# Performance work log

Hardware: AMD Instinct MI355X
Metric: run time of the kernel (lower is better)

The kernel has to match this reference:

```python
import jax, jax.numpy as jnp
import numpy as np

NUM_HEADS = 16


def setup_inputs() -> dict:
    rng = jax.random.key(0)
    ks = jax.random.split(rng, 11)
    T, B, E = 1024, 4, 1024
    s = E ** -0.5  # weight init scale
    return {
        "query": jax.random.normal(ks[0], (T, B, E), jnp.float32),
        "key": jax.random.normal(ks[1], (T, B, E), jnp.float32),
        "value": jax.random.normal(ks[2], (T, B, E), jnp.float32),
        "q_proj_weight": jax.random.normal(ks[3], (E, E), jnp.float32) * s,
        "k_proj_weight1": jax.random.normal(ks[4], (E, E), jnp.float32) * s,
        "k_proj_weight2": jax.random.normal(ks[5], (E, E), jnp.float32) * s,
        "v_proj_weight": jax.random.normal(ks[6], (E, E), jnp.float32) * s,
        "in_proj_bias": jax.random.normal(ks[7], (4 * E,), jnp.float32) * 0.02,
        "out_proj_weight": jax.random.normal(ks[8], (E, E), jnp.float32) * s,
        "out_proj_bias": jax.random.normal(ks[9], (E,), jnp.float32) * 0.02,
        "pi": jax.random.uniform(ks[10], (2, NUM_HEADS), jnp.float32, 0.3, 0.7),
    }


def reference(query, key, value, q_proj_weight, k_proj_weight1, k_proj_weight2,
              v_proj_weight, in_proj_bias, out_proj_weight, out_proj_bias, pi):
    T, Bz, E = query.shape
    H = NUM_HEADS
    hd = E // H
    scaling = hd ** -0.5

    b_q, b_k1, b_k2, b_v = jnp.split(in_proj_bias, 4)
    q = query @ q_proj_weight.T + b_q
    k1 = key @ k_proj_weight1.T + b_k1
    k2 = key @ k_proj_weight2.T + b_k2
    v = value @ v_proj_weight.T + b_v

    def heads(x):  # (S, B, E) -> (B*H, S, hd)
        S = x.shape[0]
        return x.reshape(S, Bz * H, hd).transpose(1, 0, 2)

    q, k1, k2, v = heads(q), heads(k1), heads(k2), heads(v)

    def sqdist(a, b):  # (B*H, Nt, hd), (B*H, Ns, hd) -> (B*H, Nt, Ns)
        a2 = jnp.sum(a * a, axis=-1)
        b2 = jnp.sum(b * b, axis=-1)
        ab = jnp.einsum('btd,bsd->bts', a, b)
        return a2[:, :, None] + b2[:, None, :] - 2.0 * ab

    e1 = jnp.exp(-scaling / 2.0 * sqdist(q, k1))
    e2 = jnp.exp(-3.0 * scaling / 2.0 * sqdist(q, k2))

    pi1 = jnp.clip(jnp.abs(pi[0]), 1e-6, 2.0)  # (H,)
    pi2 = jnp.clip(jnp.abs(pi[1]), 1e-6, 2.0)

    Nt, Ns = e1.shape[1], e1.shape[2]
    attn = (e1.reshape(Bz, H, Nt, Ns) * pi1[None, :, None, None]
            + e2.reshape(Bz, H, Nt, Ns) * pi2[None, :, None, None])
    attn = attn.reshape(Bz * H, Nt, Ns)
    attn = attn / (jnp.sum(attn, axis=-1, keepdims=True) + 1e-6)

    out = jnp.einsum('bts,bsd->btd', attn, v)        # (B*H, Nt, hd)
    out = out.transpose(1, 0, 2).reshape(T, Bz, E)   # (T, B, E)
    return out @ out_proj_weight.T + out_proj_bias
```

## Files before the change

### kernel.cpp

```cpp
#include <hip/hip_runtime.h>
#include <hip/hip_bf16.h>

#define T_DIM 1024
#define B_DIM 4
#define E_DIM 1024
#define H_DIM 16
#define HD    64
#define M_DIM (T_DIM * B_DIM)

typedef __hip_bfloat16 bf16;
typedef __bf16 bf16x8 __attribute__((ext_vector_type(8)));
typedef __bf16 bf16x4 __attribute__((ext_vector_type(4)));
typedef __bf16 bf16x2 __attribute__((ext_vector_type(2)));
typedef float  f32x4  __attribute__((ext_vector_type(4)));

#define P4S ((size_t)M_DIM * E_DIM)
#define P1S ((size_t)E_DIM * E_DIM)

__global__ __launch_bounds__(256) void cvt_all(
    const float* __restrict__ q, const float* __restrict__ k,
    const float* __restrict__ v, const float* __restrict__ w0,
    const float* __restrict__ w1, const float* __restrict__ w2,
    const float* __restrict__ w3, const float* __restrict__ w4,
    __bf16* __restrict__ dst)
{
  size_t i = ((size_t)blockIdx.x * 256 + threadIdx.x) * 8;
  const float* src;
  size_t off;
  if (i < P4S)            { src = q; off = i; }
  else if (i < 2 * P4S)   { src = k; off = i - P4S; }
  else if (i < 3 * P4S)   { src = v; off = i - 2 * P4S; }
  else {
    size_t j = i - 3 * P4S;
    int wsel = (int)(j >> 20);
    off = j & (P1S - 1);
    const float* ws[5] = {w0, w1, w2, w3, w4};
    src = ws[wsel];
  }
  float4 a = *(const float4*)(src + off);
  float4 b = *(const float4*)(src + off + 4);
  bf16x8 o;
  o[0] = (__bf16)a.x; o[1] = (__bf16)a.y; o[2] = (__bf16)a.z; o[3] = (__bf16)a.w;
  o[4] = (__bf16)b.x; o[5] = (__bf16)b.y; o[6] = (__bf16)b.z; o[7] = (__bf16)b.w;
  *(bf16x8*)(dst + i) = o;
}

__device__ __forceinline__ void load_lds16(const __bf16* g, __bf16* l) {
  __builtin_amdgcn_global_load_lds(
      (__attribute__((address_space(1))) void*)(void*)g,
      (__attribute__((address_space(3))) void*)l, 16, 0, 0);
}

__device__ __forceinline__ void stage_half(
    int H, const __bf16* __restrict__ X, const __bf16* __restrict__ W,
    int bm, int bn, __bf16* As, __bf16* Bs, int tid)
{
  if (H >= 64) return;
  const int T  = H >> 2;
  const int h  = H & 3;
  const int rh = (h & 1) * 128;
  const __bf16* src = (h < 2) ? X : W;
  const int rbase   = (h < 2) ? bm : bn;
  __bf16* lb = ((h < 2) ? As : Bs) + (T & 1) * 16384;
#pragma unroll
  for (int li = 0; li < 2; ++li) {
    int r  = rh + li * 64 + (tid >> 3);
    int gc = (tid & 7) ^ (r & 7);
    load_lds16(src + (size_t)(rbase + r) * E_DIM + T * 64 + gc * 8,
               lb + (rh + li * 64) * 64 + tid * 8);
  }
}

#define RD(base, row, c) \
  (*(const bf16x8*)((base) + (row) * 64 + ((((c) ^ ((row) & 7))) << 3)))

__global__ __launch_bounds__(512, 2) void proj_gemm4(
    const __bf16* __restrict__ xbase, const __bf16* __restrict__ wbase,
    const float* __restrict__ bin, __bf16* __restrict__ cbase,
    float* __restrict__ qn_g, float* __restrict__ knr_g)
{
  __shared__ __bf16 lds[65536];
  __bf16* As = lds;
  __bf16* Bs = lds + 32768;

  const int z = blockIdx.z;
  const __bf16* X = xbase + ((z == 0) ? 0 : (z == 3) ? 2 * P4S : P4S);
  const __bf16* W = wbase + (size_t)z * P1S;
  const float* bias = bin + z * E_DIM;
  __bf16* C = cbase + (size_t)z * P4S;

  const int bm = blockIdx.x * 256;
  const int bn = blockIdx.y * 256;

  const int tid  = threadIdx.x;
  const int lane = tid & 63;
  const int w    = tid >> 6;
  const int wm   = w >> 2;
  const int wn   = w & 3;
  const int mrow = lane & 15, quad = lane >> 4;

  f32x4 acc[8][4];
#pragma unroll
  for (int m = 0; m < 8; ++m)
#pragma unroll
    for (int n = 0; n < 4; ++n) acc[m][n] = (f32x4)0.0f;

#pragma unroll
  for (int H = 0; H < 5; ++H) stage_half(H, X, W, bm, bn, As, Bs, tid);
  asm volatile("s_waitcnt vmcnt(2)" ::: "memory");
  __builtin_amdgcn_s_barrier();

  bf16x8 af[4][2];
  bf16x8 bq[4][2];

#pragma unroll 2
  for (int t = 0; t < 16; ++t) {
    const __bf16* Ab = As + (t & 1) * 16384;
    const __bf16* Bb = Bs + (t & 1) * 16384;

#pragma unroll
    for (int n = 0; n < 2; ++n)
#pragma unroll
      for (int kk = 0; kk < 2; ++kk)
        bq[n][kk] = RD(Bb, wn * 64 + n * 16 + mrow, kk * 4 + quad);
#pragma unroll
    for (int m = 0; m < 4; ++m)
#pragma unroll
      for (int kk = 0; kk < 2; ++kk)
        af[m][kk] = RD(Ab, wm * 128 + m * 16 + mrow, kk * 4 + quad);
    stage_half(4 * t + 5, X, W, bm, bn, As, Bs, tid);
    __builtin_amdgcn_s_barrier();
    asm volatile("s_waitcnt lgkmcnt(0)" ::: "memory");
    __builtin_amdgcn_s_setprio(1);
#pragma unroll
    for (int kk = 0; kk < 2; ++kk)
#pragma unroll
      for (int n = 0; n < 2; ++n)
#pragma unroll
        for (int m = 0; m < 4; ++m)
          acc[m][n] = __builtin_amdgcn_mfma_f32_16x16x32_bf16(
              af[m][kk], bq[n][kk], acc[m][n], 0, 0, 0);
    __builtin_amdgcn_s_setprio(0);
    __builtin_amdgcn_s_barrier();

#pragma unroll
    for (int n = 2; n < 4; ++n)
#pragma unroll
      for (int kk = 0; kk < 2; ++kk)
        bq[n][kk] = RD(Bb, wn * 64 + n * 16 + mrow, kk * 4 + quad);
    stage_half(4 * t + 6, X, W, bm, bn, As, Bs, tid);
    __builtin_amdgcn_s_barrier();
    asm volatile("s_waitcnt lgkmcnt(0)" ::: "memory");
    __builtin_amdgcn_s_setprio(1);
#pragma unroll
    for (int kk = 0; kk < 2; ++kk)
#pragma unroll
      for (int n = 2; n < 4; ++n)
#pragma unroll
        for (int m = 0; m < 4; ++m)
          acc[m][n] = __builtin_amdgcn_mfma_f32_16x16x32_bf16(
              af[m][kk], bq[n][kk], acc[m][n], 0, 0, 0);
    __builtin_amdgcn_s_setprio(0);
    __builtin_amdgcn_s_barrier();

#pragma unroll
    for (int m = 0; m < 4; ++m)
#pragma unroll
      for (int kk = 0; kk < 2; ++kk)
        af[m][kk] = RD(Ab, wm * 128 + 64 + m * 16 + mrow, kk * 4 + quad);
    stage_half(4 * t + 7, X, W, bm, bn, As, Bs, tid);
    __builtin_amdgcn_s_barrier();
    asm volatile("s_waitcnt lgkmcnt(0)" ::: "memory");
    __builtin_amdgcn_s_setprio(1);
#pragma unroll
    for (int kk = 0; kk < 2; ++kk)
#pragma unroll
      for (int n = 0; n < 2; ++n)
#pragma unroll
        for (int m = 0; m < 4; ++m)
          acc[4 + m][n] = __builtin_amdgcn_mfma_f32_16x16x32_bf16(
              af[m][kk], bq[n][kk], acc[4 + m][n], 0, 0, 0);
    __builtin_amdgcn_s_setprio(0);
    __builtin_amdgcn_s_barrier();

    stage_half(4 * t + 8, X, W, bm, bn, As, Bs, tid);
    __builtin_amdgcn_s_barrier();
    __builtin_amdgcn_s_setprio(1);
#pragma unroll
    for (int kk = 0; kk < 2; ++kk)
#pragma unroll
      for (int n = 2; n < 4; ++n)
#pragma unroll
        for (int m = 0; m < 4; ++m)
          acc[4 + m][n] = __builtin_amdgcn_mfma_f32_16x16x32_bf16(
              af[m][kk], bq[n][kk], acc[4 + m][n], 0, 0, 0);
    __builtin_amdgcn_s_setprio(0);
    if (t < 14)       { asm volatile("s_waitcnt vmcnt(2)" ::: "memory"); }
    else if (t == 14) { asm volatile("s_waitcnt vmcnt(0)" ::: "memory"); }
    __builtin_amdgcn_s_barrier();
  }

  f32x4 ns[8];
#pragma unroll
  for (int m = 0; m < 8; ++m) ns[m] = (f32x4)0.0f;
#pragma unroll
  for (int n = 0; n < 4; ++n) {
    int col = bn + wn * 64 + n * 16 + mrow;
    float bc = bias[col];
#pragma unroll
    for (int m = 0; m < 8; ++m) {
      int rbase = bm + wm * 128 + m * 16 + quad * 4;
#pragma unroll
      for (int r = 0; r < 4; ++r) {
        __bf16 xb = (__bf16)(acc[m][n][r] + bc);
        C[(size_t)(rbase + r) * E_DIM + col] = xb;
        float xv = (float)xb;
        ns[m][r] = fmaf(xv, xv, ns[m][r]);
      }
    }
  }
  if (z < 3) {
#pragma unroll
    for (int m = 0; m < 8; ++m)
#pragma unroll
      for (int d = 1; d < 16; d <<= 1) {
        f32x4 o;
#pragma unroll
        for (int r = 0; r < 4; ++r) o[r] = __shfl_xor(ns[m][r], d, 64);
        ns[m] += o;
      }
    if (mrow == 0) {
      int hh = (bn >> 6) + wn;
#pragma unroll
      for (int m = 0; m < 8; ++m) {
        int t = (bm >> 2) + wm * 32 + m * 4 + quad;
#pragma unroll
        for (int r = 0; r < 4; ++r) {
          int bhh = r * 16 + hh;
          float v = ns[m][r];
          if (z == 0)
            qn_g[bhh * 1024 + t] = v;
          else
            knr_g[bhh * 2048 + (t >> 5) * 64 + ((z == 2) ? 32 : 0)
                  + (t & 15) * 2 + ((t >> 4) & 1)] = v;
        }
      }
    }
  }
}

template <typename TO>
__device__ __forceinline__ void gemm_body(
    const __bf16* __restrict__ X, const __bf16* __restrict__ W,
    const float* __restrict__ bias, TO* __restrict__ C,
    int bm, int bn, int Ndim, int Kdim, __bf16* As, __bf16* Bs)
{
  const int tid  = threadIdx.x;
  const int lane = tid & 63;
  const int wave = tid >> 6;
  const int wy = (wave >> 1) * 64;
  const int wx = (wave & 1) * 64;
  const int mrow = lane & 15, quad = lane >> 4;

  const int srow = tid >> 2;
  const int ke   = (tid & 3) * 8;
  const __bf16* gA0 = X + (size_t)(bm + srow)      * Kdim + ke;
  const __bf16* gA1 = X + (size_t)(bm + srow + 64) * Kdim + ke;
  const __bf16* gB0 = W + (size_t)(bn + srow)      * Kdim + ke;
  const __bf16* gB1 = W + (size_t)(bn + srow + 64) * Kdim + ke;
  __bf16* lA0 = As + tid * 8;
  __bf16* lA1 = As + (tid + 256) * 8;
  __bf16* lB0 = Bs + tid * 8;
  __bf16* lB1 = Bs + (tid + 256) * 8;

  f32x4 acc[4][4];
#pragma unroll
  for (int i = 0; i < 4; ++i)
#pragma unroll
    for (int j = 0; j < 4; ++j) acc[i][j] = (f32x4)0.0f;

  for (int k0 = 0; k0 < Kdim; k0 += 32) {
    __syncthreads();
    load_lds16(gA0 + k0, lA0);
    load_lds16(gA1 + k0, lA1);
    load_lds16(gB0 + k0, lB0);
    load_lds16(gB1 + k0, lB1);
    __syncthreads();
    bf16x8 af[4], bf[4];
#pragma unroll
    for (int i = 0; i < 4; ++i)
      af[i] = *(const bf16x8*)(As + (wy + i * 16 + mrow) * 32 + quad * 8);
#pragma unroll
    for (int j = 0; j < 4; ++j)
      bf[j] = *(const bf16x8*)(Bs + (wx + j * 16 + mrow) * 32 + quad * 8);
#pragma unroll
    for (int i = 0; i < 4; ++i)
#pragma unroll
      for (int j = 0; j < 4; ++j)
        acc[i][j] = __builtin_amdgcn_mfma_f32_16x16x32_bf16(af[i], bf[j], acc[i][j], 0, 0, 0);
  }

#pragma unroll
  for (int j = 0; j < 4; ++j) {
    int col = bn + wx + j * 16 + mrow;
    float bc = bias[col];
#pragma unroll
    for (int i = 0; i < 4; ++i) {
      int rbase = bm + wy + i * 16 + quad * 4;
#pragma unroll
      for (int r = 0; r < 4; ++r)
        C[(size_t)(rbase + r) * Ndim + col] = (TO)(acc[i][j][r] + bc);
    }
  }
}

__global__ __launch_bounds__(256) void out_gemm(
    const __bf16* __restrict__ X, const __bf16* __restrict__ W,
    const float* __restrict__ bias, float* __restrict__ C)
{
  __shared__ __bf16 As[128 * 32];
  __shared__ __bf16 Bs[128 * 32];
  gemm_body<float>(X, W, bias, C, blockIdx.x * 128, blockIdx.y * 128,
                   E_DIM, E_DIM, As, Bs);
}

__global__ __launch_bounds__(256) void vt_only(
    const __bf16* __restrict__ Vp, __bf16* __restrict__ Vt_g)
{
  __shared__ __bf16 tile[64][88];
  const int tid = threadIdx.x;
  const int bh = blockIdx.x & 63, kt = blockIdx.x >> 6;
  const int b = bh >> 4, h = bh & 15;
  {
    int s = tid >> 2, d0 = (tid & 3) * 16;
    const __bf16* src = Vp + (size_t)((kt * 64 + s) * 4 + b) * 1024 + h * 64 + d0;
    *(bf16x8*)(&tile[s][d0])     = *(const bf16x8*)(src);
    *(bf16x8*)(&tile[s][d0 + 8]) = *(const bf16x8*)(src + 8);
  }
  __syncthreads();
#pragma unroll
  for (int c = 0; c < 2; ++c) {
    int idx = tid * 2 + c;
    int d = idx >> 3, u0 = (idx & 7) * 8;
    bf16x8 o;
#pragma unroll
    for (int i = 0; i < 8; ++i) {
      int u = u0 + i;
      int s = (u >> 5) * 32 + ((u & 31) >> 1) + (u & 1) * 16;
      o[i] = tile[s][d];
    }
    *(bf16x8*)(Vt_g + ((size_t)bh * 64 + d) * 1024 + kt * 64 + u0) = o;
  }
}

__global__ __launch_bounds__(512, 4) void mgk_attn_mfma(
    const __bf16* __restrict__ Qp, const __bf16* __restrict__ K1p,
    const __bf16* __restrict__ K2p, const __bf16* __restrict__ Vt_g,
    const float* __restrict__ qn_g, const float* __restrict__ knr_g,
    const float* __restrict__ pi, __bf16* __restrict__ AO)
{
  __shared__ __bf16 lds[33280];
  __bf16* Pl = lds + 25088;

  const int bid = blockIdx.x;
  const int bh  = (bid & 7) * 8 + ((bid >> 3) & 7);
  const int qt  = bid >> 6;
  const int b = bh >> 4, h = bh & 15;
  const int tid = threadIdx.x, lane = tid & 63, w = tid >> 6;
  const int g = w >> 2, wg = w & 3;
  const int gtid = tid & 255;
  const int mrow = lane & 15, quad = lane >> 4;

  const float cl1 = 0.0625f * 1.4426950408889634f;
  const float cl2 = 0.1875f * 1.4426950408889634f;
  const float L1 = 2.0f * cl1, L2 = 2.0f * cl2;
  const float p1 = fminf(fmaxf(fabsf(pi[h]), 1e-6f), 2.0f);
  const float p2 = fminf(fmaxf(fabsf(pi[H_DIM + h]), 1e-6f), 2.0f);
  const float lp1 = __log2f(p1), lp2 = __log2f(p2);
  const int hoff = h * 64;

  bf16x8 af[2][2];
  f32x4 aq2[2];
#pragma unroll
  for (int m = 0; m < 2; ++m) {
    const __bf16* qp = Qp + (size_t)((qt * 128 + wg * 32 + m * 16 + mrow) * 4 + b) * 1024
                       + hoff + quad * 8;
    af[m][0] = *(const bf16x8*)(qp);
    af[m][1] = *(const bf16x8*)(qp + 32);
    f32x4 qnv = *(const f32x4*)(qn_g + bh * 1024 + qt * 128 + wg * 32 + m * 16 + quad * 4);
#pragma unroll
    for (int r = 0; r < 4; ++r) aq2[m][r] = fmaf(cl1 - cl2, qnv[r], lp2);
  }

  const int srK = gtid >> 3;
  const int gcK = (gtid & 7) ^ (srK & 7);
  const __bf16* gK1 = K1p + (size_t)(srK * 4 + b) * 1024 + hoff + gcK * 8;
  const __bf16* gVt = Vt_g + ((size_t)bh * 64 + (gtid >> 2)) * 1024 + (gtid & 3) * 8;
  const float*  gkn = knr_g + bh * 2048 + wg * 16 + lane * 4;

#define STAGE_T(i_, bsel_) do {                                               \
    __bf16* bb_ = lds + (bsel_) * 6272;                                       \
    int kt_ = g * 16 + (i_);                                                  \
    load_lds16(gK1 + (size_t)kt_ * 131072,       bb_ + gtid * 8);             \
    load_lds16(gK1 + P4S + (size_t)kt_ * 131072, bb_ + 2048 + gtid * 8);      \
    load_lds16(gVt + kt_ * 32,                   bb_ + 4096 + gtid * 8);      \
    if (lane < 4)                                                             \
      load_lds16((const __bf16*)(gkn + kt_ * 64),                             \
                 bb_ + 6144 + wg * 32 + lane * 8);                            \
  } while (0)

  STAGE_T(0, g * 2);
  STAGE_T(1, g * 2 + 1);
  asm volatile("s_waitcnt vmcnt(4)" ::: "memory");
  __builtin_amdgcn_s_barrier();

  f32x4 oacc[2][4];
#pragma unroll
  for (int m = 0; m < 2; ++m)
#pragma unroll
    for (int j = 0; j < 4; ++j) oacc[m][j] = (f32x4)0.0f;
  f32x4 rsl[2] = {(f32x4)0.0f, (f32x4)0.0f};

  for (int i = 0; i < 16; ++i) {
    __bf16* buf = lds + (g * 2 + (i & 1)) * 6272;
    const __bf16* K1s = buf;
    const __bf16* K2s = buf + 2048;
    const __bf16* Vts = buf + 4096;
    const float*  knb = (const float*)(buf + 6144);

    float2 f1 = *(const float2*)(knb + mrow * 2);
    float2 f2 = *(const float2*)(knb + 32 + mrow * 2);
    float nb1[2], s2v[2];
    nb1[0] = fmaf(-cl1, f1.x, lp1); nb1[1] = fmaf(-cl1, f1.y, lp1);
    s2v[0] = -cl2 * f2.x;           s2v[1] = -cl2 * f2.y;

    f32x4 acc1[2][2], acc2[2][2];
#pragma unroll
    for (int m = 0; m < 2; ++m)
#pragma unroll
      for (int j = 0; j < 2; ++j) { acc1[m][j] = (f32x4)0.0f; acc2[m][j] = (f32x4)0.0f; }
    __builtin_amdgcn_s_setprio(1);
#pragma unroll
    for (int kk = 0; kk < 2; ++kk)
#pragma unroll
      for (int j = 0; j < 2; ++j) {
        int row = j * 16 + mrow;
        int off = row * 64 + (((kk * 4 + quad) ^ (row & 7)) << 3);
        bf16x8 b1f = *(const bf16x8*)(K1s + off);
        bf16x8 b2f = *(const bf16x8*)(K2s + off);
#pragma unroll
        for (int m = 0; m < 2; ++m) {
          acc1[m][j] = __builtin_amdgcn_mfma_f32_16x16x32_bf16(af[m][kk], b1f, acc1[m][j], 0, 0, 0);
          acc2[m][j] = __builtin_amdgcn_mfma_f32_16x16x32_bf16(af[m][kk], b2f, acc2[m][j], 0, 0, 0);
        }
      }
    __builtin_amdgcn_s_setprio(0);

#pragma unroll
    for (int m = 0; m < 2; ++m) {
      f32x4 pj[2];
#pragma unroll
      for (int j = 0; j < 2; ++j) {
        f32x4 p;
#pragma unroll
        for (int r = 0; r < 4; ++r) {
          float e1 = __builtin_amdgcn_exp2f(fmaf(L1, acc1[m][j][r], nb1[j]));
          float e2 = __builtin_amdgcn_exp2f(fmaf(L2, acc2[m][j][r], s2v[j] + aq2[m][r]));
          p[r] = e1 + e2;
        }
        pj[j] = p;
        rsl[m] += p;
      }
#pragma unroll
      for (int r = 0; r < 4; ++r) {
        int q = m * 16 + quad * 4 + r;
        bf16x2 pk; pk[0] = (__bf16)pj[0][r]; pk[1] = (__bf16)pj[1][r];
        *(bf16x2*)(Pl + w * 1024 + q * 32 + mrow * 2) = pk;
      }
    }

    bf16x8 pf[2];
#pragma unroll
    for (int m = 0; m < 2; ++m)
      pf[m] = *(const bf16x8*)(Pl + w * 1024 + (m * 16 + mrow) * 32 + quad * 8);
    __builtin_amdgcn_s_setprio(1);
#pragma unroll
    for (int j = 0; j < 4; ++j) {
      bf16x8 vf = *(const bf16x8*)(Vts + (j * 16 + mrow) * 32 + quad * 8);
#pragma unroll
      for (int m = 0; m < 2; ++m)
        oacc[m][j] = __builtin_amdgcn_mfma_f32_16x16x32_bf16(pf[m], vf, oacc[m][j], 0, 0, 0);
    }
    __builtin_amdgcn_s_setprio(0);

    if (i < 15) {
      asm volatile("s_waitcnt lgkmcnt(0)" ::: "memory");
      __builtin_amdgcn_s_barrier();
      if (i < 14) {
        STAGE_T(i + 2, g * 2 + (i & 1));
        asm volatile("s_waitcnt vmcnt(4)" ::: "memory");
      } else {
        asm volatile("s_waitcnt vmcnt(0)" ::: "memory");
      }
      __builtin_amdgcn_s_barrier();
    }
  }
#undef STAGE_T

  __builtin_amdgcn_s_barrier();
  float* Of = (float*)lds;
  float* Rf = (float*)Pl;
  if (g == 1) {
#pragma unroll
    for (int m = 0; m < 2; ++m) {
#pragma unroll
      for (int j = 0; j < 4; ++j)
#pragma unroll
        for (int r = 0; r < 4; ++r)
          Of[(wg * 32 + m * 16 + quad * 4 + r) * 64 + j * 16 + mrow] = oacc[m][j][r];
#pragma unroll
      for (int r = 0; r < 4; ++r)
        Rf[(wg * 32 + m * 16 + quad * 4 + r) * 16 + mrow] = rsl[m][r];
    }
  }
  __builtin_amdgcn_s_barrier();
  if (g == 0) {
#pragma unroll
    for (int m = 0; m < 2; ++m) {
#pragma unroll
      for (int j = 0; j < 4; ++j)
#pragma unroll
        for (int r = 0; r < 4; ++r)
          oacc[m][j][r] += Of[(wg * 32 + m * 16 + quad * 4 + r) * 64 + j * 16 + mrow];
#pragma unroll
      for (int r = 0; r < 4; ++r)
        rsl[m][r] += Rf[(wg * 32 + m * 16 + quad * 4 + r) * 16 + mrow];
    }
#pragma unroll
    for (int m = 0; m < 2; ++m) {
#pragma unroll
      for (int d = 1; d < 16; d <<= 1) {
        f32x4 o;
#pragma unroll
        for (int r = 0; r < 4; ++r) o[r] = __shfl_xor(rsl[m][r], d, 64);
        rsl[m] += o;
      }
      f32x4 inv;
#pragma unroll
      for (int r = 0; r < 4; ++r) inv[r] = 1.0f / (rsl[m][r] + 1e-6f);
#pragma unroll
      for (int j = 0; j < 4; ++j) {
        int col = hoff + j * 16 + mrow;
#pragma unroll
        for (int r = 0; r < 4; ++r) {
          int t = qt * 128 + wg * 32 + m * 16 + quad * 4 + r;
          AO[(size_t)(t * 4 + b) * 1024 + col] = (__bf16)(oacc[m][j][r] * inv[r]);
        }
      }
    }
  }
}

extern "C" void kernel_launch(void* const* d_in, const int* in_sizes, int n_in,
                              void* d_out, int out_size, void* d_ws, size_t ws_size,
                              hipStream_t stream) {
  const float* query = (const float*)d_in[0];
  const float* key   = (const float*)d_in[1];
  const float* value = (const float*)d_in[2];
  const float* Wq    = (const float*)d_in[3];
  const float* Wk1   = (const float*)d_in[4];
  const float* Wk2   = (const float*)d_in[5];
  const float* Wv    = (const float*)d_in[6];
  const float* bin   = (const float*)d_in[7];
  const float* Wo    = (const float*)d_in[8];
  const float* bo    = (const float*)d_in[9];
  const float* pi    = (const float*)d_in[10];
  float* out = (float*)d_out;

  __bf16* qc  = (__bf16*)d_ws;
  __bf16* wq  = qc  + 3 * P4S;
  __bf16* wo  = wq  + 4 * P1S;
  __bf16* Qp  = wq  + 5 * P1S;
  __bf16* K1p = Qp  + P4S;
  __bf16* K2p = K1p + P4S;
  __bf16* Vp  = K2p + P4S;
  __bf16* AO  = Vp  + P4S;
  float*  qn_g = (float*)(AO + P4S);
  float*  knr  = qn_g + 64 * 1024;
  __bf16* Vt_g = qc;

  cvt_all<<<8704, 256, 0, stream>>>(query, key, value, Wq, Wk1, Wk2, Wv, Wo, qc);

  proj_gemm4<<<dim3(M_DIM / 256, E_DIM / 256, 4), 512, 0, stream>>>(
      qc, wq, bin, Qp, qn_g, knr);

  vt_only<<<1024, 256, 0, stream>>>(Vp, Vt_g);

  mgk_attn_mfma<<<512, 512, 0, stream>>>(
      Qp, K1p, K2p, Vt_g, qn_g, knr, pi, AO);

  out_gemm<<<dim3(M_DIM / 128, E_DIM / 128), 256, 0, stream>>>(AO, wo, bo, out);
}
```

Measured before the change: 264.3 us.

## Drop split-KV wave groups in attention; one 256-thread group walks all keys

The attention kernel previously ran 512 threads as two wave groups, each handling half of the key tiles, then merged partial outputs and row sums through LDS. It now uses 256 threads that iterate over all 32 key tiles, which removes the cross-group reduction and halves LDS usage. It also preloads all key norms once into LDS and adds XOR swizzling to the P and V tile layouts to cut bank conflicts. The trade-off is fewer waves per block and a serial loop twice as long, so there is less latency hiding inside each block unless occupancy rises to compensate.

```diff
diff --git a/kernel.cpp b/kernel.cpp
--- a/kernel.cpp
+++ b/kernel.cpp
@@ -353,22 +353,21 @@
   }
 }
 
-__global__ __launch_bounds__(512, 4) void mgk_attn_mfma(
+__global__ __launch_bounds__(256, 2) void mgk_attn_mfma(
     const __bf16* __restrict__ Qp, const __bf16* __restrict__ K1p,
     const __bf16* __restrict__ K2p, const __bf16* __restrict__ Vt_g,
     const float* __restrict__ qn_g, const float* __restrict__ knr_g,
     const float* __restrict__ pi, __bf16* __restrict__ AO)
 {
-  __shared__ __bf16 lds[33280];
-  __bf16* Pl = lds + 25088;
+  __shared__ __bf16 lds[20480];
+  __bf16* Pl  = lds + 12288;
+  float*  knl = (float*)(lds + 16384);
 
   const int bid = blockIdx.x;
   const int bh  = (bid & 7) * 8 + ((bid >> 3) & 7);
   const int qt  = bid >> 6;
   const int b = bh >> 4, h = bh & 15;
   const int tid = threadIdx.x, lane = tid & 63, w = tid >> 6;
-  const int g = w >> 2, wg = w & 3;
-  const int gtid = tid & 255;
   const int mrow = lane & 15, quad = lane >> 4;
 
   const float cl1 = 0.0625f * 1.4426950408889634f;
@@ -383,35 +382,39 @@
   f32x4 aq2[2];
 #pragma unroll
   for (int m = 0; m < 2; ++m) {
-    const __bf16* qp = Qp + (size_t)((qt * 128 + wg * 32 + m * 16 + mrow) * 4 + b) * 1024
+    const __bf16* qp = Qp + (size_t)((qt * 128 + w * 32 + m * 16 + mrow) * 4 + b) * 1024
                        + hoff + quad * 8;
     af[m][0] = *(const bf16x8*)(qp);
     af[m][1] = *(const bf16x8*)(qp + 32);
-    f32x4 qnv = *(const f32x4*)(qn_g + bh * 1024 + qt * 128 + wg * 32 + m * 16 + quad * 4);
+    f32x4 qnv = *(const f32x4*)(qn_g + bh * 1024 + qt * 128 + w * 32 + m * 16 + quad * 4);
 #pragma unroll
     for (int r = 0; r < 4; ++r) aq2[m][r] = fmaf(cl1 - cl2, qnv[r], lp2);
   }
 
-  const int srK = gtid >> 3;
-  const int gcK = (gtid & 7) ^ (srK & 7);
-  const __bf16* gK1 = K1p + (size_t)(srK * 4 + b) * 1024 + hoff + gcK * 8;
-  const __bf16* gVt = Vt_g + ((size_t)bh * 64 + (gtid >> 2)) * 1024 + (gtid & 3) * 8;
-  const float*  gkn = knr_g + bh * 2048 + wg * 16 + lane * 4;
-
-#define STAGE_T(i_, bsel_) do {                                               \
-    __bf16* bb_ = lds + (bsel_) * 6272;                                       \
-    int kt_ = g * 16 + (i_);                                                  \
-    load_lds16(gK1 + (size_t)kt_ * 131072,       bb_ + gtid * 8);             \
-    load_lds16(gK1 + P4S + (size_t)kt_ * 131072, bb_ + 2048 + gtid * 8);      \
-    load_lds16(gVt + kt_ * 32,                   bb_ + 4096 + gtid * 8);      \
-    if (lane < 4)                                                             \
-      load_lds16((const __bf16*)(gkn + kt_ * 64),                             \
-                 bb_ + 6144 + wg * 32 + lane * 8);                            \
+  const int srow = tid >> 3;
+  const int pch  = tid & 7;
+  const int gcK  = pch ^ (srow & 7);
+  const __bf16* gK1 = K1p + (size_t)(srow * 4 + b) * 1024 + hoff + gcK * 8;
+  const __bf16* gK2 = K2p + (size_t)(srow * 4 + b) * 1024 + hoff + gcK * 8;
+  const int vcl = pch ^ (srow & 7);
+  const int vd  = (vcl >> 2) * 32 + srow;
+  const int vu0 = (vcl & 3) * 8;
+  const __bf16* gVt = Vt_g + ((size_t)bh * 64 + vd) * 1024 + vu0;
+
+#define STAGE_T(kt_, bsel_) do {                                              \
+    __bf16* bb_ = lds + (bsel_) * 6144;                                       \
+    load_lds16(gK1 + (size_t)(kt_) * 131072, bb_ + tid * 8);                  \
+    load_lds16(gK2 + (size_t)(kt_) * 131072, bb_ + 2048 + tid * 8);           \
+    load_lds16(gVt + (kt_) * 32,             bb_ + 4096 + tid * 8);           \
   } while (0)
 
-  STAGE_T(0, g * 2);
-  STAGE_T(1, g * 2 + 1);
-  asm volatile("s_waitcnt vmcnt(4)" ::: "memory");
+  load_lds16((const __bf16*)(knr_g + bh * 2048 + tid * 4),
+             (__bf16*)knl + tid * 8);
+  load_lds16((const __bf16*)(knr_g + bh * 2048 + 1024 + tid * 4),
+             (__bf16*)knl + 2048 + tid * 8);
+  STAGE_T(0, 0);
+  STAGE_T(1, 1);
+  asm volatile("s_waitcnt vmcnt(3)" ::: "memory");
   __builtin_amdgcn_s_barrier();
 
   f32x4 oacc[2][4];
@@ -421,15 +424,14 @@
     for (int j = 0; j < 4; ++j) oacc[m][j] = (f32x4)0.0f;
   f32x4 rsl[2] = {(f32x4)0.0f, (f32x4)0.0f};
 
-  for (int i = 0; i < 16; ++i) {
-    __bf16* buf = lds + (g * 2 + (i & 1)) * 6272;
+  for (int i = 0; i < 32; ++i) {
+    const __bf16* buf = lds + (i & 1) * 6144;
     const __bf16* K1s = buf;
     const __bf16* K2s = buf + 2048;
     const __bf16* Vts = buf + 4096;
-    const float*  knb = (const float*)(buf + 6144);
-
-    float2 f1 = *(const float2*)(knb + mrow * 2);
-    float2 f2 = *(const float2*)(knb + 32 + mrow * 2);
+
+    float2 f1 = *(const float2*)(knl + i * 64 + mrow * 2);
+    float2 f2 = *(const float2*)(knl + i * 64 + 32 + mrow * 2);
     float nb1[2], s2v[2];
     nb1[0] = fmaf(-cl1, f1.x, lp1); nb1[1] = fmaf(-cl1, f1.y, lp1);
     s2v[0] = -cl2 * f2.x;           s2v[1] = -cl2 * f2.y;
@@ -473,32 +475,36 @@
       }
 #pragma unroll
       for (int r = 0; r < 4; ++r) {
-        int q = m * 16 + quad * 4 + r;
+        int row  = quad * 4 + r;
+        int phys = (m * 4 + (mrow >> 2)) ^ (row & 7);
         bf16x2 pk; pk[0] = (__bf16)pj[0][r]; pk[1] = (__bf16)pj[1][r];
-        *(bf16x2*)(Pl + w * 1024 + q * 32 + mrow * 2) = pk;
+        *(bf16x2*)(Pl + w * 1024 + row * 64 + phys * 8 + (mrow & 3) * 2) = pk;
       }
     }
 
     bf16x8 pf[2];
 #pragma unroll
     for (int m = 0; m < 2; ++m)
-      pf[m] = *(const bf16x8*)(Pl + w * 1024 + (m * 16 + mrow) * 32 + quad * 8);
+      pf[m] = *(const bf16x8*)(Pl + w * 1024 + mrow * 64
+                               + (((m * 4 + quad) ^ (mrow & 7)) << 3));
     __builtin_amdgcn_s_setprio(1);
 #pragma unroll
     for (int j = 0; j < 4; ++j) {
-      bf16x8 vf = *(const bf16x8*)(Vts + (j * 16 + mrow) * 32 + quad * 8);
+      int rowv = (j & 1) * 16 + mrow;
+      int cl   = (j >> 1) * 4 + quad;
+      bf16x8 vf = *(const bf16x8*)(Vts + rowv * 64 + ((cl ^ (rowv & 7)) << 3));
 #pragma unroll
       for (int m = 0; m < 2; ++m)
         oacc[m][j] = __builtin_amdgcn_mfma_f32_16x16x32_bf16(pf[m], vf, oacc[m][j], 0, 0, 0);
     }
     __builtin_amdgcn_s_setprio(0);
 
-    if (i < 15) {
+    if (i < 31) {
       asm volatile("s_waitcnt lgkmcnt(0)" ::: "memory");
       __builtin_amdgcn_s_barrier();
-      if (i < 14) {
-        STAGE_T(i + 2, g * 2 + (i & 1));
-        asm volatile("s_waitcnt vmcnt(4)" ::: "memory");
+      if (i < 30) {
+        STAGE_T(i + 2, i & 1);
+        asm volatile("s_waitcnt vmcnt(3)" ::: "memory");
       } else {
         asm volatile("s_waitcnt vmcnt(0)" ::: "memory");
       }
@@ -507,55 +513,25 @@
   }
 #undef STAGE_T
 
-  __builtin_amdgcn_s_barrier();
-  float* Of = (float*)lds;
-  float* Rf = (float*)Pl;
-  if (g == 1) {
-#pragma unroll
-    for (int m = 0; m < 2; ++m) {
-#pragma unroll
-      for (int j = 0; j < 4; ++j)
-#pragma unroll
-        for (int r = 0; r < 4; ++r)
-          Of[(wg * 32 + m * 16 + quad * 4 + r) * 64 + j * 16 + mrow] = oacc[m][j][r];
-#pragma unroll
-      for (int r = 0; r < 4; ++r)
-        Rf[(wg * 32 + m * 16 + quad * 4 + r) * 16 + mrow] = rsl[m][r];
-    }
-  }
-  __builtin_amdgcn_s_barrier();
-  if (g == 0) {
-#pragma unroll
-    for (int m = 0; m < 2; ++m) {
-#pragma unroll
-      for (int j = 0; j < 4; ++j)
-#pragma unroll
-        for (int r = 0; r < 4; ++r)
-          oacc[m][j][r] += Of[(wg * 32 + m * 16 + quad * 4 + r) * 64 + j * 16 + mrow];
-#pragma unroll
-      for (int r = 0; r < 4; ++r)
-        rsl[m][r] += Rf[(wg * 32 + m * 16 + quad * 4 + r) * 16 + mrow];
-    }
-#pragma unroll
-    for (int m = 0; m < 2; ++m) {
-#pragma unroll
-      for (int d = 1; d < 16; d <<= 1) {
-        f32x4 o;
-#pragma unroll
-        for (int r = 0; r < 4; ++r) o[r] = __shfl_xor(rsl[m][r], d, 64);
-        rsl[m] += o;
-      }
-      f32x4 inv;
-#pragma unroll
-      for (int r = 0; r < 4; ++r) inv[r] = 1.0f / (rsl[m][r] + 1e-6f);
-#pragma unroll
-      for (int j = 0; j < 4; ++j) {
-        int col = hoff + j * 16 + mrow;
-#pragma unroll
-        for (int r = 0; r < 4; ++r) {
-          int t = qt * 128 + wg * 32 + m * 16 + quad * 4 + r;
-          AO[(size_t)(t * 4 + b) * 1024 + col] = (__bf16)(oacc[m][j][r] * inv[r]);
-        }
+#pragma unroll
+  for (int m = 0; m < 2; ++m) {
+#pragma unroll
+    for (int d = 1; d < 16; d <<= 1) {
+      f32x4 o;
+#pragma unroll
+      for (int r = 0; r < 4; ++r) o[r] = __shfl_xor(rsl[m][r], d, 64);
+      rsl[m] += o;
+    }
+    f32x4 inv;
+#pragma unroll
+    for (int r = 0; r < 4; ++r) inv[r] = 1.0f / (rsl[m][r] + 1e-6f);
+#pragma unroll
+    for (int j = 0; j < 4; ++j) {
+      int col = hoff + j * 16 + mrow;
+#pragma unroll
+      for (int r = 0; r < 4; ++r) {
+        int t = qt * 128 + w * 32 + m * 16 + quad * 4 + r;
+        AO[(size_t)(t * 4 + b) * 1024 + col] = (__bf16)(oacc[m][j][r] * inv[r]);
       }
     }
   }
@@ -596,7 +572,7 @@
 
   vt_only<<<1024, 256, 0, stream>>>(Vp, Vt_g);
 
-  mgk_attn_mfma<<<512, 512, 0, stream>>>(
+  mgk_attn_mfma<<<512, 256, 0, stream>>>(
       Qp, K1p, K2p, Vt_g, qn_g, knr, pi, AO);
 
   out_gemm<<<dim3(M_DIM / 128, E_DIM / 128), 256, 0, stream>>>(AO, wo, bo, out);
```

Measured after the change: 246.1 us. 1.07x faster.

## Swizzle P and V LDS tiles, preload key norms once, relax launch bounds

Applied to the files above, without the earlier changes.

Adds XOR swizzles to the P scratch tile and the V tile in LDS so the MFMA operand reads avoid bank conflicts. The per-tile key-norm loads are replaced by a single upfront load of all key norms into a dedicated LDS region, which removes one async load per stage and adjusts the vmcnt waits to match. K2 now gets its own pointer instead of an offset from K1, and launch bounds drop from 4 to 2 blocks per CU, giving the compiler more registers at the cost of possible occupancy.

```diff
diff --git a/kernel.cpp b/kernel.cpp
--- a/kernel.cpp
+++ b/kernel.cpp
@@ -353,14 +353,15 @@
   }
 }
 
-__global__ __launch_bounds__(512, 4) void mgk_attn_mfma(
+__global__ __launch_bounds__(512, 2) void mgk_attn_mfma(
     const __bf16* __restrict__ Qp, const __bf16* __restrict__ K1p,
     const __bf16* __restrict__ K2p, const __bf16* __restrict__ Vt_g,
     const float* __restrict__ qn_g, const float* __restrict__ knr_g,
     const float* __restrict__ pi, __bf16* __restrict__ AO)
 {
-  __shared__ __bf16 lds[33280];
-  __bf16* Pl = lds + 25088;
+  __shared__ __bf16 lds[36864];
+  __bf16* Pl  = lds + 24576;
+  float*  knl = (float*)(lds + 32768);
 
   const int bid = blockIdx.x;
   const int bh  = (bid & 7) * 8 + ((bid >> 3) & 7);
@@ -392,26 +393,29 @@
     for (int r = 0; r < 4; ++r) aq2[m][r] = fmaf(cl1 - cl2, qnv[r], lp2);
   }
 
-  const int srK = gtid >> 3;
-  const int gcK = (gtid & 7) ^ (srK & 7);
-  const __bf16* gK1 = K1p + (size_t)(srK * 4 + b) * 1024 + hoff + gcK * 8;
-  const __bf16* gVt = Vt_g + ((size_t)bh * 64 + (gtid >> 2)) * 1024 + (gtid & 3) * 8;
-  const float*  gkn = knr_g + bh * 2048 + wg * 16 + lane * 4;
+  const int srow = gtid >> 3;
+  const int pch  = gtid & 7;
+  const int gcK  = pch ^ (srow & 7);
+  const __bf16* gK1 = K1p + (size_t)(srow * 4 + b) * 1024 + hoff + gcK * 8;
+  const __bf16* gK2 = K2p + (size_t)(srow * 4 + b) * 1024 + hoff + gcK * 8;
+  const int vcl = pch ^ (srow & 7);
+  const int vd  = (vcl >> 2) * 32 + srow;
+  const int vu0 = (vcl & 3) * 8;
+  const __bf16* gVt = Vt_g + ((size_t)bh * 64 + vd) * 1024 + vu0;
 
 #define STAGE_T(i_, bsel_) do {                                               \
-    __bf16* bb_ = lds + (bsel_) * 6272;                                       \
+    __bf16* bb_ = lds + (bsel_) * 6144;                                       \
     int kt_ = g * 16 + (i_);                                                  \
-    load_lds16(gK1 + (size_t)kt_ * 131072,       bb_ + gtid * 8);             \
-    load_lds16(gK1 + P4S + (size_t)kt_ * 131072, bb_ + 2048 + gtid * 8);      \
-    load_lds16(gVt + kt_ * 32,                   bb_ + 4096 + gtid * 8);      \
-    if (lane < 4)                                                             \
-      load_lds16((const __bf16*)(gkn + kt_ * 64),                             \
-                 bb_ + 6144 + wg * 32 + lane * 8);                            \
+    load_lds16(gK1 + (size_t)kt_ * 131072, bb_ + gtid * 8);                   \
+    load_lds16(gK2 + (size_t)kt_ * 131072, bb_ + 2048 + gtid * 8);            \
+    load_lds16(gVt + kt_ * 32,             bb_ + 4096 + gtid * 8);            \
   } while (0)
 
+  load_lds16((const __bf16*)(knr_g + bh * 2048 + tid * 4),
+             (__bf16*)knl + tid * 8);
   STAGE_T(0, g * 2);
   STAGE_T(1, g * 2 + 1);
-  asm volatile("s_waitcnt vmcnt(4)" ::: "memory");
+  asm volatile("s_waitcnt vmcnt(3)" ::: "memory");
   __builtin_amdgcn_s_barrier();
 
   f32x4 oacc[2][4];
@@ -422,14 +426,14 @@
   f32x4 rsl[2] = {(f32x4)0.0f, (f32x4)0.0f};
 
   for (int i = 0; i < 16; ++i) {
-    __bf16* buf = lds + (g * 2 + (i & 1)) * 6272;
+    const __bf16* buf = lds + (g * 2 + (i & 1)) * 6144;
     const __bf16* K1s = buf;
     const __bf16* K2s = buf + 2048;
     const __bf16* Vts = buf + 4096;
-    const float*  knb = (const float*)(buf + 6144);
-
-    float2 f1 = *(const float2*)(knb + mrow * 2);
-    float2 f2 = *(const float2*)(knb + 32 + mrow * 2);
+
+    const float* knt = knl + (g * 16 + i) * 64;
+    float2 f1 = *(const float2*)(knt + mrow * 2);
+    float2 f2 = *(const float2*)(knt + 32 + mrow * 2);
     float nb1[2], s2v[2];
     nb1[0] = fmaf(-cl1, f1.x, lp1); nb1[1] = fmaf(-cl1, f1.y, lp1);
     s2v[0] = -cl2 * f2.x;           s2v[1] = -cl2 * f2.y;
@@ -473,20 +477,24 @@
       }
 #pragma unroll
       for (int r = 0; r < 4; ++r) {
-        int q = m * 16 + quad * 4 + r;
+        int row  = quad * 4 + r;
+        int phys = (m * 4 + (mrow >> 2)) ^ (row & 7);
         bf16x2 pk; pk[0] = (__bf16)pj[0][r]; pk[1] = (__bf16)pj[1][r];
-        *(bf16x2*)(Pl + w * 1024 + q * 32 + mrow * 2) = pk;
+        *(bf16x2*)(Pl + w * 1024 + row * 64 + phys * 8 + (mrow & 3) * 2) = pk;
       }
     }
 
     bf16x8 pf[2];
 #pragma unroll
     for (int m = 0; m < 2; ++m)
-      pf[m] = *(const bf16x8*)(Pl + w * 1024 + (m * 16 + mrow) * 32 + quad * 8);
+      pf[m] = *(const bf16x8*)(Pl + w * 1024 + mrow * 64
+                               + (((m * 4 + quad) ^ (mrow & 7)) << 3));
     __builtin_amdgcn_s_setprio(1);
 #pragma unroll
     for (int j = 0; j < 4; ++j) {
-      bf16x8 vf = *(const bf16x8*)(Vts + (j * 16 + mrow) * 32 + quad * 8);
+      int rowv = (j & 1) * 16 + mrow;
+      int cl   = (j >> 1) * 4 + quad;
+      bf16x8 vf = *(const bf16x8*)(Vts + rowv * 64 + ((cl ^ (rowv & 7)) << 3));
 #pragma unroll
       for (int m = 0; m < 2; ++m)
         oacc[m][j] = __builtin_amdgcn_mfma_f32_16x16x32_bf16(pf[m], vf, oacc[m][j], 0, 0, 0);
@@ -498,7 +506,7 @@
       __builtin_amdgcn_s_barrier();
       if (i < 14) {
         STAGE_T(i + 2, g * 2 + (i & 1));
-        asm volatile("s_waitcnt vmcnt(4)" ::: "memory");
+        asm volatile("s_waitcnt vmcnt(3)" ::: "memory");
       } else {
         asm volatile("s_waitcnt vmcnt(0)" ::: "memory");
       }
```

Result: faster. 246.8 us (-6.6%).
